# Performance work log

Measured on AMD Instinct MI355X. Metric: run time of the kernel, lower is better.

The kernel has to match this reference:

```python
import jax, jax.numpy as jnp
import numpy as np

# --- SLAYER-style constants (network.yaml defaults) ---
T_BINS = 350      # tSample / Ts
TS = 1.0          # simulation time step
THETA = 10.0      # spike threshold
TAU_SR = 10.0     # SRM (psp) kernel time constant
TAU_REF = 1.0     # refractory kernel time constant
SCALE_REF = 2.0
TAU_RHO = 1.0     # surrogate-gradient width (unused in fwd)
SCALE_RHO = 1.0
REF_LEN = 32      # truncated refractory kernel length
B = 32            # batch

_t = jnp.arange(T_BINS, dtype=jnp.float32) * TS
SRM_KERNEL = (_t / TAU_SR) * jnp.exp(1.0 - _t / TAU_SR)            # alpha kernel, peak 1 at t=tauSr
_tr = jnp.arange(REF_LEN, dtype=jnp.float32) * TS
REF_KERNEL = -SCALE_REF * THETA * (_tr / TAU_REF) * jnp.exp(1.0 - _tr / TAU_REF)


def psp(x):
    # causal temporal convolution with SRM kernel; x: [B, N, T]
    b, n, t = x.shape
    k = SRM_KERNEL[::-1].reshape(1, 1, T_BINS)  # flip: lax conv is cross-correlation
    y = jax.lax.conv_general_dilated(x.reshape(b * n, 1, t), k, (1,), [(T_BINS - 1, 0)])
    return y.reshape(b, n, t)


def _spike_fwd_impl(u):
    # threshold + refractory dynamics, serial over time; u: [B, N, T]
    uT = jnp.moveaxis(u, -1, 0)  # [T, B, N]
    def step(buf, ut):
        v = ut + buf[..., 0]                       # membrane + pending refractory
        s = (v >= THETA).astype(u.dtype)           # 0/1 spike indicator
        buf = jnp.concatenate([buf[..., 1:], jnp.zeros_like(buf[..., :1])], axis=-1) \
              + s[..., None] * REF_KERNEL
        return buf, s / TS
    buf0 = jnp.zeros(u.shape[:-1] + (REF_LEN,), u.dtype)
    _, sT = jax.lax.scan(step, buf0, uT)
    return jnp.moveaxis(sT, 0, -1)


@jax.custom_vjp
def spike(u):
    return _spike_fwd_impl(u)

def _spike_f(u):
    return _spike_fwd_impl(u), u

def _spike_b(u, g):
    # SLAYER surrogate gradient: pdf of spiking
    pdf = (SCALE_RHO / TAU_RHO) * jnp.exp(-jnp.abs(u - THETA) / TAU_RHO)
    return (g * pdf,)

spike.defvjp(_spike_f, _spike_b)


def encode(inp, table):
    # vectorized pixel->time-bin one-hot scatter (replaces the Python quadruple loop)
    t_idx = table[inp]                                   # gather: [B,3,32,32]
    return jax.nn.one_hot(t_idx, T_BINS, dtype=jnp.float32) / TS  # [B,3,32,32,T]


def setup_inputs() -> dict:
    key = jax.random.key(0)
    k1, k2, k3 = jax.random.split(key, 3)
    inp = jax.random.randint(k1, (B, 3, 32, 32), 0, 256, dtype=jnp.int32)
    table = ((jnp.arange(256) * T_BINS) // 256).astype(jnp.int32)  # pixel value -> time bin
    w1 = jax.random.normal(k2, (240, 3 * 32 * 32), dtype=jnp.float32)
    w2 = jax.random.normal(k3, (10, 240), dtype=jnp.float32)
    return {"inp": inp, "table": table, "w1": w1, "w2": w2}


def reference(inp, table, w1, w2):
    spikes = encode(inp, table).reshape(inp.shape[0], -1, T_BINS)      # [B,3072,T]
    l1 = spike(psp(jnp.einsum('bpt,np->bnt', spikes, w1)))             # [B,240,T]
    l2 = spike(psp(jnp.einsum('bpt,np->bnt', l1, w2)))                 # [B,10,T]
    return l2
```

## Files before the change

kernel.cpp:

```cpp
#include <hip/hip_runtime.h>
#include <math.h>

#define T_BINS 350
#define REF_LEN 32
#define NB 32
#define NPIX 3072
#define N1 240
#define N2 10
#define NVAL 256

__global__ void prep(const int* __restrict__ inp,
                     int* __restrict__ pix,
                     int* __restrict__ offs,
                     int* __restrict__ cnts,
                     const float* __restrict__ w1,
                     float* __restrict__ w1t,
                     const int* __restrict__ table,
                     int* __restrict__ inv)
{
    __shared__ int lc[NVAL];
    __shared__ int ls[NVAL];
    __shared__ int lslot[NVAL];
    __shared__ float tile[64][65];
    __shared__ int linv[T_BINS];

    const int tid = threadIdx.x;

    if (blockIdx.x < NB) {
        const int b = blockIdx.x;
        lc[tid] = 0;
        __syncthreads();

        int vals[12];
        #pragma unroll
        for (int i = 0; i < 12; ++i) {
            int v = inp[b * NPIX + i * 256 + tid];
            vals[i] = v;
            atomicAdd(&lc[v], 1);
        }
        __syncthreads();

        int x = lc[tid];
        ls[tid] = x;
        __syncthreads();
        for (int d = 1; d < 256; d <<= 1) {
            int y = (tid >= d) ? ls[tid - d] : 0;
            __syncthreads();
            ls[tid] += y;
            __syncthreads();
        }
        int excl = ls[tid] - x;
        offs[b * NVAL + tid] = excl;
        cnts[b * NVAL + tid] = x;
        lslot[tid] = excl;
        __syncthreads();

        #pragma unroll
        for (int i = 0; i < 12; ++i) {
            int slot = atomicAdd(&lslot[vals[i]], 1);
            pix[b * NPIX + slot] = i * 256 + tid;
        }
    } else if (blockIdx.x < NB + 192) {
        const int tt = blockIdx.x - NB;
        const int p0 = (tt % 48) * 64;
        const int n0 = (tt / 48) * 64;
        const int c  = tid & 63;
        const int r0 = tid >> 6;

        #pragma unroll
        for (int i = 0; i < 16; ++i) {
            int n = n0 + r0 + i * 4;
            if (n < N1) tile[r0 + i * 4][c] = w1[n * NPIX + p0 + c];
        }
        __syncthreads();
        #pragma unroll
        for (int i = 0; i < 16; ++i) {
            int p = p0 + r0 + i * 4;
            int n = n0 + c;
            if (n < N1) w1t[p * N1 + n] = tile[c][r0 + i * 4];
        }
    } else {
        for (int i = tid; i < T_BINS; i += 256) linv[i] = -1;
        __syncthreads();
        if (tid < NVAL) linv[table[tid]] = tid;
        __syncthreads();
        for (int i = tid; i < T_BINS; i += 256) inv[i] = linv[i];
    }
}

__global__ void compute_u1(const float* __restrict__ w1t,
                           const int* __restrict__ pix,
                           const int* __restrict__ offs,
                           const int* __restrict__ cnts,
                           const int* __restrict__ inv,
                           double* __restrict__ u1t)
{
    __shared__ int lpix[NPIX];
    const int t = blockIdx.x;
    const int b = blockIdx.y;
    const int tid = threadIdx.x;
    const int v = inv[t];

    double acc = 0.0;
    if (v >= 0) {
        const int cnt = cnts[b * NVAL + v];
        const int off = offs[b * NVAL + v];
        const int* pl = pix + b * NPIX + off;
        for (int i = tid; i < cnt; i += 256) lpix[i] = pl[i];
        __syncthreads();
        if (tid < N1)
            for (int i = 0; i < cnt; ++i)
                acc += (double)w1t[lpix[i] * N1 + tid];
    }
    if (tid < N1)
        u1t[((size_t)b * T_BINS + t) * N1 + tid] = acc;
}

#define DYN_CONSTS \
    const double A    = 0.9048374180359595;     \
    const double C    = 0.2718281828459045;     \
    const double Ar   = 0.36787944117144233;    \
    const double Cr   = -54.365636569180904;    \
    const double C31A = 1.0671679036256927e-12; \
    const double C31B = 3.4424771084699765e-14;

#define DYN_STEP(uin, sout)                                   \
    {                                                         \
        q = A * (q + p);                                      \
        p = A * p + (uin);                                    \
        double vm = C * q + Cr * Q;                           \
        unsigned int sb = (vm >= 10.0) ? 1u : 0u;             \
        double s = (double)sb;                                \
        double sel31 = (hist & 0x80000000u) ? C31A : 0.0;     \
        double sel30 = (hist & 0x40000000u) ? C31B : 0.0;     \
        Q = Ar * (Q + P - sel31);                             \
        P = s + (Ar * P - sel30);                             \
        hist = (hist << 1) | sb;                              \
        (sout) = (float)s;                                    \
    }

__global__ __launch_bounds__(64) void layer1_dyn(
                           const double* __restrict__ u1t,
                           float* __restrict__ s1)
{
    const int tid = threadIdx.x;
    const int b   = blockIdx.x >> 2;
    const int n   = (blockIdx.x & 3) * 64 + tid;
    if (n >= N1) return;

    const double* ub = u1t + (size_t)b * T_BINS * N1 + n;
    float*        sp = s1 + (size_t)b * T_BINS * N1 + n;

    DYN_CONSTS
    double p = 0.0, q = 0.0, P = 0.0, Q = 0.0;
    unsigned int hist = 0u;

    double cb[10], nb[10];
    #pragma unroll
    for (int i = 0; i < 10; ++i) cb[i] = ub[(size_t)i * N1];

    for (int t0 = 0; t0 < T_BINS; t0 += 10) {
        if (t0 + 10 < T_BINS) {
            #pragma unroll
            for (int i = 0; i < 10; ++i) nb[i] = ub[(size_t)(t0 + 10 + i) * N1];
        }
        #pragma unroll
        for (int i = 0; i < 10; ++i)
            DYN_STEP(cb[i], sp[(size_t)(t0 + i) * N1]);
        #pragma unroll
        for (int i = 0; i < 10; ++i) cb[i] = nb[i];
    }
}

__global__ void compute_u2(const float* __restrict__ s1,
                           const float* __restrict__ w2,
                           double* __restrict__ u2)
{
    int id = blockIdx.x * 256 + threadIdx.x;
    if (id >= NB * T_BINS * N2) return;
    int bt = id / N2;
    int m  = id - bt * N2;
    const float4* s4 = (const float4*)(s1 + (size_t)bt * N1);
    const float4* w4 = (const float4*)(w2 + m * N1);
    double a0 = 0.0, a1 = 0.0;
    #pragma unroll 4
    for (int i = 0; i < N1 / 4; ++i) {
        float4 sv = s4[i];
        float4 wv = w4[i];
        a0 += (double)sv.x * (double)wv.x + (double)sv.y * (double)wv.y;
        a1 += (double)sv.z * (double)wv.z + (double)sv.w * (double)wv.w;
    }
    u2[id] = a0 + a1;
}

__global__ void layer2_dyn(const double* __restrict__ u2,
                           float* __restrict__ out)
{
    const int id = blockIdx.x * 64 + threadIdx.x;
    if (id >= NB * N2) return;
    const int b = id / N2;
    const int m = id - b * N2;
    const double* up = u2 + (size_t)b * T_BINS * N2 + m;
    float*        op = out + ((size_t)b * N2 + m) * T_BINS;

    DYN_CONSTS
    double p = 0.0, q = 0.0, P = 0.0, Q = 0.0;
    unsigned int hist = 0u;

    double cb[14], nb[14];
    #pragma unroll
    for (int i = 0; i < 14; ++i) cb[i] = up[(size_t)i * N2];

    for (int t0 = 0; t0 < T_BINS; t0 += 14) {
        if (t0 + 14 < T_BINS) {
            #pragma unroll
            for (int i = 0; i < 14; ++i) nb[i] = up[(size_t)(t0 + 14 + i) * N2];
        }
        #pragma unroll
        for (int i = 0; i < 14; ++i)
            DYN_STEP(cb[i], op[t0 + i]);
        #pragma unroll
        for (int i = 0; i < 14; ++i) cb[i] = nb[i];
    }
}

extern "C" void kernel_launch(void* const* d_in, const int* in_sizes, int n_in,
                              void* d_out, int out_size, void* d_ws, size_t ws_size,
                              hipStream_t stream) {
    const int*   inp   = (const int*)d_in[0];
    const int*   table = (const int*)d_in[1];
    const float* w1    = (const float*)d_in[2];
    const float* w2    = (const float*)d_in[3];
    float* out = (float*)d_out;

    char* ws = (char*)d_ws;
    size_t off = 0;
    double* u1t = (double*)(ws + off); off += (size_t)NB * T_BINS * N1 * 8;
    double* u2  = (double*)(ws + off); off += (size_t)NB * T_BINS * N2 * 8;
    float* w1t  = (float*)(ws + off);  off += (size_t)NPIX * N1 * 4;
    float* s1   = (float*)(ws + off);  off += (size_t)NB * T_BINS * N1 * 4;
    int*   pix  = (int*)(ws + off);    off += (size_t)NB * NPIX * 4;
    int*  offs  = (int*)(ws + off);    off += (size_t)NB * NVAL * 4;
    int*  cnts  = (int*)(ws + off);    off += (size_t)NB * NVAL * 4;
    int*   inv  = (int*)(ws + off);    off += (size_t)T_BINS * 4;

    prep<<<NB + 192 + 1, 256, 0, stream>>>(inp, pix, offs, cnts, w1, w1t, table, inv);
    compute_u1<<<dim3(T_BINS, NB), 256, 0, stream>>>(w1t, pix, offs, cnts, inv, u1t);
    layer1_dyn<<<NB * 4, 64, 0, stream>>>(u1t, s1);
    compute_u2<<<(NB * T_BINS * N2 + 255) / 256, 256, 0, stream>>>(s1, w2, u2);
    layer2_dyn<<<(NB * N2 + 63) / 64, 64, 0, stream>>>(u2, out);
}
```

Baseline: 155.6 us.

## Bit-pack layer-1 spikes with ballot masks and sparse-sum layer-2 inputs

Layer-1 spikes are stored as 64-bit wavefront ballot masks instead of a dense float array, and compute_u2 iterates only over set bits, summing w2 entries held in shared memory. This cuts s1 traffic and the dense 240-wide dot product per output. compute_u1 also drops the shared-memory staging and barrier, reading pixel indices directly with 4-way unrolled loads. Accumulation order inside the double sums changes slightly. On the final k=3 block only 48 lanes are active, so the upper ballot bits are zero.

```diff
diff --git a/kernel.cpp b/kernel.cpp
--- a/kernel.cpp
+++ b/kernel.cpp
@@ -95,25 +95,29 @@
                            const int* __restrict__ inv,
                            double* __restrict__ u1t)
 {
-    __shared__ int lpix[NPIX];
     const int t = blockIdx.x;
     const int b = blockIdx.y;
     const int tid = threadIdx.x;
+    if (tid >= N1) return;
     const int v = inv[t];
 
     double acc = 0.0;
     if (v >= 0) {
         const int cnt = cnts[b * NVAL + v];
-        const int off = offs[b * NVAL + v];
-        const int* pl = pix + b * NPIX + off;
-        for (int i = tid; i < cnt; i += 256) lpix[i] = pl[i];
-        __syncthreads();
-        if (tid < N1)
-            for (int i = 0; i < cnt; ++i)
-                acc += (double)w1t[lpix[i] * N1 + tid];
-    }
-    if (tid < N1)
-        u1t[((size_t)b * T_BINS + t) * N1 + tid] = acc;
+        const int* pl = pix + b * NPIX + offs[b * NVAL + v];
+        int i = 0;
+        for (; i + 4 <= cnt; i += 4) {
+            int p0 = pl[i], p1 = pl[i + 1], p2 = pl[i + 2], p3 = pl[i + 3];
+            double w0 = (double)w1t[p0 * N1 + tid];
+            double w1v = (double)w1t[p1 * N1 + tid];
+            double w2v = (double)w1t[p2 * N1 + tid];
+            double w3 = (double)w1t[p3 * N1 + tid];
+            acc += w0; acc += w1v; acc += w2v; acc += w3;
+        }
+        for (; i < cnt; ++i)
+            acc += (double)w1t[pl[i] * N1 + tid];
+    }
+    u1t[((size_t)b * T_BINS + t) * N1 + tid] = acc;
 }
 
 #define DYN_CONSTS \
@@ -124,8 +128,7 @@
     const double C31A = 1.0671679036256927e-12; \
     const double C31B = 3.4424771084699765e-14;
 
-#define DYN_STEP(uin, sout)                                   \
-    {                                                         \
+#define DYN_CORE(uin)                                         \
         q = A * (q + p);                                      \
         p = A * p + (uin);                                    \
         double vm = C * q + Cr * Q;                           \
@@ -135,21 +138,20 @@
         double sel30 = (hist & 0x40000000u) ? C31B : 0.0;     \
         Q = Ar * (Q + P - sel31);                             \
         P = s + (Ar * P - sel30);                             \
-        hist = (hist << 1) | sb;                              \
-        (sout) = (float)s;                                    \
-    }
+        hist = (hist << 1) | sb;
 
 __global__ __launch_bounds__(64) void layer1_dyn(
                            const double* __restrict__ u1t,
-                           float* __restrict__ s1)
+                           unsigned long long* __restrict__ s1m)
 {
     const int tid = threadIdx.x;
     const int b   = blockIdx.x >> 2;
-    const int n   = (blockIdx.x & 3) * 64 + tid;
+    const int k   = blockIdx.x & 3;
+    const int n   = k * 64 + tid;
     if (n >= N1) return;
 
     const double* ub = u1t + (size_t)b * T_BINS * N1 + n;
-    float*        sp = s1 + (size_t)b * T_BINS * N1 + n;
+    unsigned long long* mp = s1m + ((size_t)b * T_BINS) * 4 + k;
 
     DYN_CONSTS
     double p = 0.0, q = 0.0, P = 0.0, Q = 0.0;
@@ -165,32 +167,42 @@
             for (int i = 0; i < 10; ++i) nb[i] = ub[(size_t)(t0 + 10 + i) * N1];
         }
         #pragma unroll
-        for (int i = 0; i < 10; ++i)
-            DYN_STEP(cb[i], sp[(size_t)(t0 + i) * N1]);
+        for (int i = 0; i < 10; ++i) {
+            DYN_CORE(cb[i])
+            unsigned long long msk = __ballot(sb != 0u);
+            if (tid == 0) mp[(size_t)(t0 + i) * 4] = msk;
+        }
         #pragma unroll
         for (int i = 0; i < 10; ++i) cb[i] = nb[i];
     }
 }
 
-__global__ void compute_u2(const float* __restrict__ s1,
+__global__ void compute_u2(const unsigned long long* __restrict__ s1m,
                            const float* __restrict__ w2,
                            double* __restrict__ u2)
 {
-    int id = blockIdx.x * 256 + threadIdx.x;
+    __shared__ float lw2[N2][N1];
+    const int tid = threadIdx.x;
+    for (int i = tid; i < N2 * N1; i += 256) lw2[i / N1][i % N1] = w2[i];
+    __syncthreads();
+
+    int id = blockIdx.x * 256 + tid;
     if (id >= NB * T_BINS * N2) return;
     int bt = id / N2;
     int m  = id - bt * N2;
-    const float4* s4 = (const float4*)(s1 + (size_t)bt * N1);
-    const float4* w4 = (const float4*)(w2 + m * N1);
-    double a0 = 0.0, a1 = 0.0;
-    #pragma unroll 4
-    for (int i = 0; i < N1 / 4; ++i) {
-        float4 sv = s4[i];
-        float4 wv = w4[i];
-        a0 += (double)sv.x * (double)wv.x + (double)sv.y * (double)wv.y;
-        a1 += (double)sv.z * (double)wv.z + (double)sv.w * (double)wv.w;
-    }
-    u2[id] = a0 + a1;
+    const unsigned long long* mp = s1m + (size_t)bt * 4;
+
+    double acc = 0.0;
+    #pragma unroll
+    for (int kk = 0; kk < 4; ++kk) {
+        unsigned long long msk = mp[kk];
+        while (msk) {
+            int j = __ffsll(msk) - 1;
+            acc += (double)lw2[m][kk * 64 + j];
+            msk &= msk - 1;
+        }
+    }
+    u2[id] = acc;
 }
 
 __global__ void layer2_dyn(const double* __restrict__ u2,
@@ -217,8 +229,10 @@
             for (int i = 0; i < 14; ++i) nb[i] = up[(size_t)(t0 + 14 + i) * N2];
         }
         #pragma unroll
-        for (int i = 0; i < 14; ++i)
-            DYN_STEP(cb[i], op[t0 + i]);
+        for (int i = 0; i < 14; ++i) {
+            DYN_CORE(cb[i])
+            op[t0 + i] = (float)s;
+        }
         #pragma unroll
         for (int i = 0; i < 14; ++i) cb[i] = nb[i];
     }
@@ -238,7 +252,8 @@
     double* u1t = (double*)(ws + off); off += (size_t)NB * T_BINS * N1 * 8;
     double* u2  = (double*)(ws + off); off += (size_t)NB * T_BINS * N2 * 8;
     float* w1t  = (float*)(ws + off);  off += (size_t)NPIX * N1 * 4;
-    float* s1   = (float*)(ws + off);  off += (size_t)NB * T_BINS * N1 * 4;
+    unsigned long long* s1m = (unsigned long long*)(ws + off);
+    off += (size_t)NB * T_BINS * 4 * 8;
     int*   pix  = (int*)(ws + off);    off += (size_t)NB * NPIX * 4;
     int*  offs  = (int*)(ws + off);    off += (size_t)NB * NVAL * 4;
     int*  cnts  = (int*)(ws + off);    off += (size_t)NB * NVAL * 4;
@@ -246,7 +261,7 @@
 
     prep<<<NB + 192 + 1, 256, 0, stream>>>(inp, pix, offs, cnts, w1, w1t, table, inv);
     compute_u1<<<dim3(T_BINS, NB), 256, 0, stream>>>(w1t, pix, offs, cnts, inv, u1t);
-    layer1_dyn<<<NB * 4, 64, 0, stream>>>(u1t, s1);
-    compute_u2<<<(NB * T_BINS * N2 + 255) / 256, 256, 0, stream>>>(s1, w2, u2);
+    layer1_dyn<<<NB * 4, 64, 0, stream>>>(u1t, s1m);
+    compute_u2<<<(NB * T_BINS * N2 + 255) / 256, 256, 0, stream>>>(s1m, w2, u2);
     layer2_dyn<<<(NB * N2 + 63) / 64, 64, 0, stream>>>(u2, out);
 }
```

Result: no change. 154.8 us (-0.5%).
